# Kernel tuning notes

Hardware: AMD Instinct MI355X
Metric: run time of the kernel (lower is better)

Reference implementation:

```python
import jax, jax.numpy as jnp
import numpy as np

B, S, D = 4, 2048, 512
H, DK, DV = 8, 64, 64


def setup_inputs() -> dict:
    key = jax.random.key(0)
    ks = jax.random.split(key, 12)
    inv = 1.0 / np.sqrt(D)
    return {
        "query": jax.random.normal(ks[0], (B, S, D), dtype=jnp.float32),
        "value": jax.random.normal(ks[1], (B, S, D), dtype=jnp.float32),
        "attention_mask": jax.random.randint(ks[2], (B, S), 0, 2, dtype=jnp.int32),
        "Wq": jax.random.normal(ks[3], (D, H * DK), dtype=jnp.float32) * inv,
        "bq": jnp.zeros((H * DK,), dtype=jnp.float32),
        "Wk": jax.random.normal(ks[4], (D, H * DK), dtype=jnp.float32) * inv,
        "bk": jnp.zeros((H * DK,), dtype=jnp.float32),
        "Wv": jax.random.normal(ks[5], (D, H * DV), dtype=jnp.float32) * inv,
        "bv": jnp.zeros((H * DV,), dtype=jnp.float32),
        "Wo": jax.random.normal(ks[6], (H * DV, D), dtype=jnp.float32) * inv,
        "bo": jnp.zeros((D,), dtype=jnp.float32),
    }


def _split_heads(x, h):
    b, s, _ = x.shape
    return x.reshape(b, s, h, -1).transpose(0, 2, 1, 3)  # (B,H,S,dh)


def reference(query, value, attention_mask, Wq, bq, Wk, bk, Wv, bv, Wo, bo):
    # QKV projections (activation=None -> identity); key defaults to value
    q = _split_heads(query @ Wq + bq, H)   # (B,H,S,DK)
    k = _split_heads(value @ Wk + bk, H)   # (B,H,S,DK)
    v = _split_heads(value @ Wv + bv, H)   # (B,H,S,DV)

    scores = jnp.einsum("bhqd,bhkd->bhqk", q, k) / jnp.sqrt(jnp.float32(DK))
    # additive mask: m = 1e9*(mask-1), applied on both key and query axes
    m = 1e9 * (attention_mask.astype(jnp.float32) - 1.0)  # (B,S)
    scores = scores + m[:, None, None, :] + m[:, None, :, None]

    weights = jax.nn.softmax(scores, axis=-1)
    ctx = jnp.einsum("bhqk,bhkd->bhqd", weights, v)        # (B,H,S,DV)
    ctx = ctx.transpose(0, 2, 1, 3).reshape(ctx.shape[0], ctx.shape[2], H * DV)
    return ctx @ Wo + bo  # (B,S,D)
```

## Files before the change

### kernel.cpp

```cpp
#include <hip/hip_runtime.h>

#define B_ 4
#define S_ 2048
#define D_ 512
#define H_ 8

typedef __attribute__((ext_vector_type(8))) __bf16 bf16x8;
typedef __attribute__((ext_vector_type(4))) float f32x4;

#define NEGBIG  -1.442695040e9f
#define QSCALE  0.18033688011112042f

__device__ __forceinline__ unsigned pack_rn(float a, float b) {
    union { float f; unsigned u; } ua, ub; ua.f = a; ub.f = b;
    return __builtin_amdgcn_perm(ub.u + 0x8000u, ua.u + 0x8000u, 0x07060302u);
}

__device__ __forceinline__ void gl16(const void* g, void* l) {
    __builtin_amdgcn_global_load_lds(
        (const __attribute__((address_space(1))) unsigned int*)g,
        (__attribute__((address_space(3))) unsigned int*)l, 16, 0, 0);
}

__global__ __launch_bounds__(256) void pre_all(
    const float* __restrict__ q, const float* __restrict__ v,
    const int* __restrict__ am,
    const float* __restrict__ Wq, const float* __restrict__ Wk,
    const float* __restrict__ Wv, const float* __restrict__ Wo,
    unsigned short* __restrict__ xq, unsigned short* __restrict__ xv,
    unsigned short* __restrict__ Tq, unsigned short* __restrict__ Tk,
    unsigned short* __restrict__ Tv, unsigned short* __restrict__ To,
    int* __restrict__ idxc, int* __restrict__ nvout,
    float* __restrict__ Mf, float* __restrict__ Mc)
{
    const int bid = blockIdx.x;
    const int tid = threadIdx.x;

    if (bid < 4096) {
        const int z = bid >> 11, xb = bid & 2047;
        const float* src = z ? v : q;
        unsigned short* dst = z ? xv : xq;
        int i = (xb * 256 + tid) * 8;
        float4 f0 = *(const float4*)&src[i];
        float4 f1 = *(const float4*)&src[i + 4];
        uint4 o;
        o.x = pack_rn(f0.x, f0.y); o.y = pack_rn(f0.z, f0.w);
        o.z = pack_rn(f1.x, f1.y); o.w = pack_rn(f1.z, f1.w);
        *(uint4*)&dst[i] = o;
    } else if (bid < 4352) {
        int r = bid - 4096;
        int z = r >> 6, rem = r & 63;
        const float* W = (z == 0) ? Wq : (z == 1) ? Wk : (z == 2) ? Wv : Wo;
        unsigned short* T = (z == 0) ? Tq : (z == 1) ? Tk : (z == 2) ? Tv : To;
        int n0 = (rem & 7) * 64, k0 = (rem >> 3) * 64;

        __shared__ float Ts[64][69];
        #pragma unroll
        for (int it = 0; it < 4; it++) {
            int lin = tid + it * 256;
            int kr = lin >> 4, c4 = (lin & 15) * 4;
            float4 vv = *(const float4*)&W[(k0 + kr) * 512 + n0 + c4];
            Ts[kr][c4 + 0] = vv.x; Ts[kr][c4 + 1] = vv.y;
            Ts[kr][c4 + 2] = vv.z; Ts[kr][c4 + 3] = vv.w;
        }
        __syncthreads();
        int n = tid >> 2, kc = tid & 3;
        unsigned p[8];
        #pragma unroll
        for (int j = 0; j < 8; j++)
            p[j] = pack_rn(Ts[kc * 16 + 2 * j][n], Ts[kc * 16 + 2 * j + 1][n]);
        unsigned short* dst = &T[(n0 + n) * 512 + k0 + kc * 16];
        *(uint4*)dst       = *(uint4*)&p[0];
        *(uint4*)(dst + 8) = *(uint4*)&p[4];
    } else {
        const int w = tid >> 6, lane = tid & 63;
        const int* amb = am + w * 2048;
        int m[32];
        #pragma unroll
        for (int s = 0; s < 32; s++) m[s] = amb[s * 64 + lane];

        int* ib = idxc + w * 2048;
        const unsigned long long lt = (1ULL << lane) - 1ULL;
        int base = 0;
        #pragma unroll
        for (int s = 0; s < 32; s++) {
            unsigned long long bal = __ballot(m[s] != 0);
            if (m[s]) ib[base + __popcll(bal & lt)] = s * 64 + lane;
            base += __popcll(bal);
        }
        const int nv = base;
        for (int i = nv + lane; i < 2048; i += 64) ib[i] = 0;
        float* mfb = Mf + w * 2048;
        float* mcb = Mc + w * 2048;
        #pragma unroll
        for (int s = 0; s < 32; s++) {
            int i = s * 64 + lane;
            mfb[i] = m[s] ? 0.f : NEGBIG;
            mcb[i] = (i < nv) ? 0.f : NEGBIG;
        }
        if (lane == 0) nvout[w] = nv;
    }
}

__global__ __launch_bounds__(256) void proj_qkv_mfma(
    const unsigned short* __restrict__ Xq, const unsigned short* __restrict__ Xv,
    const unsigned short* __restrict__ Wtq, const unsigned short* __restrict__ Wtk,
    const unsigned short* __restrict__ Wtv,
    const float* __restrict__ bq, const float* __restrict__ bk,
    const float* __restrict__ bv,
    const int* __restrict__ idxc, const int* __restrict__ nv1,
    unsigned short* __restrict__ Qb, unsigned short* __restrict__ Kb,
    unsigned short* __restrict__ VtG)
{
    const int z = blockIdx.z;
    const unsigned short* A  = (z == 0) ? Wtq : (z == 1) ? Wtk : Xv;
    const unsigned short* Bm = (z == 0) ? Xq  : (z == 1) ? Xv  : Wtv;
    const float* bias        = (z == 0) ? bq  : (z == 1) ? bk  : bv;
    const int m0 = (z < 2) ? blockIdx.y * 128 : blockIdx.x * 128;
    const int n0 = (z < 2) ? blockIdx.x * 128 : blockIdx.y * 128;

    if (z == 1) {
        int bb = n0 >> 11, cap = (nv1[bb] + 127) & ~127;
        if (cap < 128) cap = 128;
        if ((n0 & 2047) >= cap) return;
    }
    if (z == 2) {
        int bb = m0 >> 11, cap = (nv1[bb] + 127) & ~127;
        if (cap < 128) cap = 128;
        if ((m0 & 2047) >= cap) return;
    }

    const int tid = threadIdx.x;
    const int w = tid >> 6, lane = tid & 63;
    const int l15 = lane & 15, quad = lane >> 4;
    const int wm = (w >> 1) * 64, wn = (w & 1) * 64;

    __shared__ unsigned short As[128 * 64];
    __shared__ unsigned short Bs[128 * 64];

    const int srw  = tid >> 3;
    const int csrc = (tid & 7) ^ (srw & 7);
    const unsigned short* aS[4];
    const unsigned short* bS[4];
    unsigned short* la[4];
    unsigned short* lb[4];
    #pragma unroll
    for (int is = 0; is < 4; is++) {
        int ra = m0 + is * 32 + srw;
        int rb = n0 + is * 32 + srw;
        long sa = ra, sb = rb;
        if (z == 2) { int bb = ra >> 11; sa = (long)bb * 2048 + idxc[bb * 2048 + (ra & 2047)]; }
        if (z == 1) { int bb = rb >> 11; sb = (long)bb * 2048 + idxc[bb * 2048 + (rb & 2047)]; }
        aS[is] = A  + sa * 512 + csrc * 8;
        bS[is] = Bm + sb * 512 + csrc * 8;
        la[is] = &As[is * 2048 + w * 512];
        lb[is] = &Bs[is * 2048 + w * 512];
    }

    const int koff0 = ((quad    ) ^ (l15 & 7)) * 8;
    const int koff1 = ((quad + 4) ^ (l15 & 7)) * 8;

    f32x4 acc[4][4];
    #pragma unroll
    for (int i = 0; i < 4; i++)
        #pragma unroll
        for (int j = 0; j < 4; j++) acc[i][j] = (f32x4){0.f, 0.f, 0.f, 0.f};

    for (int k0 = 0; k0 < 512; k0 += 64) {
        __syncthreads();
        #pragma unroll
        for (int is = 0; is < 4; is++) {
            gl16(aS[is] + k0, la[is]);
            gl16(bS[is] + k0, lb[is]);
        }
        __syncthreads();
        #pragma unroll
        for (int kc = 0; kc < 2; kc++) {
            const int ko = kc ? koff1 : koff0;
            bf16x8 a[4], bb[4];
            #pragma unroll
            for (int i = 0; i < 4; i++)
                a[i] = *(const bf16x8*)&As[(wm + 16 * i + l15) * 64 + ko];
            #pragma unroll
            for (int j = 0; j < 4; j++)
                bb[j] = *(const bf16x8*)&Bs[(wn + 16 * j + l15) * 64 + ko];
            #pragma unroll
            for (int i = 0; i < 4; i++)
                #pragma unroll
                for (int j = 0; j < 4; j++)
                    acc[i][j] = __builtin_amdgcn_mfma_f32_16x16x32_bf16(a[i], bb[j], acc[i][j], 0, 0, 0);
        }
    }

    if (z == 2) {
        #pragma unroll
        for (int j = 0; j < 4; j++) {
            int N = n0 + wn + 16 * j + l15;
            float bv_ = bias[N];
            int h = N >> 6, d = N & 63;
            #pragma unroll
            for (int i = 0; i < 4; i++) {
                int Mb = m0 + wm + 16 * i + quad * 4;
                int b = Mb >> 11, s = Mb & 2047;
                uint2 o;
                o.x = pack_rn(acc[i][j][0] + bv_, acc[i][j][1] + bv_);
                o.y = pack_rn(acc[i][j][2] + bv_, acc[i][j][3] + bv_);
                *(uint2*)&VtG[((b * H_ + h) * 64 + d) * 2048 + s] = o;
            }
        }
    } else {
        unsigned short* dst = (z == 0) ? Qb : Kb;
        const float scale = (z == 0) ? QSCALE : 1.0f;
        #pragma unroll
        for (int j = 0; j < 4; j++) {
            int sg = n0 + wn + 16 * j + l15;
            int b = sg >> 11, s = sg & 2047;
            #pragma unroll
            for (int i = 0; i < 4; i++) {
                int F = m0 + wm + 16 * i + quad * 4;
                int h = F >> 6, d = F & 63;
                float4 b4 = *(const float4*)&bias[F];
                uint2 o;
                o.x = pack_rn((acc[i][j][0] + b4.x) * scale, (acc[i][j][1] + b4.y) * scale);
                o.y = pack_rn((acc[i][j][2] + b4.z) * scale, (acc[i][j][3] + b4.w) * scale);
                *(uint2*)&dst[((b * H_ + h) * 2048 + s) * 64 + d] = o;
            }
        }
    }
}

__global__ __launch_bounds__(256, 2) void flash_mfma(
    const unsigned short* __restrict__ Qg, const unsigned short* __restrict__ Kg,
    const unsigned short* __restrict__ VtG, const float* __restrict__ Mf,
    const float* __restrict__ Mc, const int* __restrict__ nvalid,
    unsigned short* __restrict__ ctxB)
{
    const int bid = blockIdx.x;
    const int xcd = bid & 7, idx = bid >> 3;
    const int bh = xcd * 4 + (idx & 3);
    const int q0 = (idx >> 2) * 128;
    const int b = bh >> 3, h = bh & 7;

    const int tid = threadIdx.x;
    const int w = tid >> 6, lane = tid & 63;
    const int l15 = lane & 15, quad = lane >> 4;
    const int swz = l15 & 7;

    __shared__ unsigned short Ks[2][64 * 64];
    __shared__ unsigned short Ps[4][32 * 64];
    unsigned short* pw = &Ps[w][0];

    const int nv = nvalid[b];
    int ntiles = (nv + 63) >> 6;
    if (ntiles < 1) ntiles = 1;

    const float* mfb = Mf + b * 2048;
    const float* mcp = Mc + b * 2048 + quad * 4;

    bf16x8 qf[2][2];
    float mq[2];
    #pragma unroll
    for (int qb = 0; qb < 2; qb++) {
        int qrow = q0 + w * 32 + qb * 16 + l15;
        const unsigned short* p = &Qg[((long)bh * 2048 + qrow) * 64 + quad * 8];
        qf[qb][0] = *(const bf16x8*)p;
        qf[qb][1] = *(const bf16x8*)(p + 32);
        mq[qb] = mfb[qrow];
    }

    const unsigned short* vp[4];
    #pragma unroll
    for (int i = 0; i < 4; i++)
        vp[i] = VtG + ((long)bh * 64 + i * 16 + l15) * 2048 + quad * 8;

    const int srow = tid >> 2;
    const int sch  = (tid & 3) * 2;
    const unsigned short* kgb = Kg + (long)bh * 2048 * 64;
    const int sw0 = srow * 64 + ((sch    ) ^ (srow & 7)) * 8;
    const int sw1 = srow * 64 + ((sch + 1) ^ (srow & 7)) * 8;

    {
        uint4 a = *(const uint4*)&kgb[srow * 64 + sch * 8];
        uint4 c = *(const uint4*)&kgb[srow * 64 + sch * 8 + 8];
        *(uint4*)&Ks[0][sw0] = a;
        *(uint4*)&Ks[0][sw1] = c;
    }

    const int koff0 = ((quad    ) ^ swz) * 8;
    const int koff1 = ((quad + 4) ^ swz) * 8;

    f32x4 accO[2][4];
    #pragma unroll
    for (int qb = 0; qb < 2; qb++)
        #pragma unroll
        for (int dt = 0; dt < 4; dt++) accO[qb][dt] = (f32x4){0.f, 0.f, 0.f, 0.f};
    float mi[2] = {-3.0e38f, -3.0e38f};
    float li[2] = {0.f, 0.f};

    __syncthreads();

    for (int t = 0; t < ntiles; t++) {
        const int kt = t * 64;
        const int ktn = (t + 1 < ntiles) ? kt + 64 : kt;
        const int cur = t & 1, nxt = cur ^ 1;

        bf16x8 vf[4][2];
        #pragma unroll
        for (int dt = 0; dt < 4; dt++) {
            vf[dt][0] = *(const bf16x8*)(vp[dt] + kt);
            vf[dt][1] = *(const bf16x8*)(vp[dt] + kt + 32);
        }
        uint4 kst0 = *(const uint4*)&kgb[(ktn + srow) * 64 + sch * 8];
        uint4 kst1 = *(const uint4*)&kgb[(ktn + srow) * 64 + sch * 8 + 8];
        f32x4 kmf[4];
        #pragma unroll
        for (int nt = 0; nt < 4; nt++)
            kmf[nt] = *(const f32x4*)(mcp + kt + nt * 16);

        bf16x8 kf[4][2];
        #pragma unroll
        for (int nt = 0; nt < 4; nt++) {
            kf[nt][0] = *(const bf16x8*)&Ks[cur][(nt * 16 + l15) * 64 + koff0];
            kf[nt][1] = *(const bf16x8*)&Ks[cur][(nt * 16 + l15) * 64 + koff1];
        }
        f32x4 sc[2][4];
        #pragma unroll
        for (int qb = 0; qb < 2; qb++)
            #pragma unroll
            for (int nt = 0; nt < 4; nt++) {
                f32x4 c = kmf[nt];
                c[0] += mq[qb]; c[1] += mq[qb]; c[2] += mq[qb]; c[3] += mq[qb];
                sc[qb][nt] = c;
            }
        __builtin_amdgcn_s_setprio(1);
        #pragma unroll
        for (int qb = 0; qb < 2; qb++)
            #pragma unroll
            for (int nt = 0; nt < 4; nt++) {
                sc[qb][nt] = __builtin_amdgcn_mfma_f32_16x16x32_bf16(
                    kf[nt][0], qf[qb][0], sc[qb][nt], 0, 0, 0);
                sc[qb][nt] = __builtin_amdgcn_mfma_f32_16x16x32_bf16(
                    kf[nt][1], qf[qb][1], sc[qb][nt], 0, 0, 0);
            }
        __builtin_amdgcn_s_setprio(0);

        #pragma unroll
        for (int qb = 0; qb < 2; qb++) {
            float mloc = fmaxf(fmaxf(sc[qb][0][0], sc[qb][0][1]),
                               fmaxf(sc[qb][0][2], sc[qb][0][3]));
            #pragma unroll
            for (int nt = 1; nt < 4; nt++)
                mloc = fmaxf(mloc, fmaxf(fmaxf(sc[qb][nt][0], sc[qb][nt][1]),
                                         fmaxf(sc[qb][nt][2], sc[qb][nt][3])));
            mloc = fmaxf(mloc, __shfl_xor(mloc, 16));
            mloc = fmaxf(mloc, __shfl_xor(mloc, 32));

            float mn = mi[qb];
            if (!__all(mloc <= mn + 4.f)) {
                float mo = mn;
                mn = fmaxf(mo, mloc);
                float alpha = __builtin_amdgcn_exp2f(mo - mn);
                li[qb] *= alpha;
                #pragma unroll
                for (int dt = 0; dt < 4; dt++) {
                    accO[qb][dt][0] *= alpha; accO[qb][dt][1] *= alpha;
                    accO[qb][dt][2] *= alpha; accO[qb][dt][3] *= alpha;
                }
                mi[qb] = mn;
            }

            float ps = 0.f;
            const int prbase = (qb * 16 + l15) * 64;
            #pragma unroll
            for (int nt = 0; nt < 4; nt++) {
                float p0 = __builtin_amdgcn_exp2f(sc[qb][nt][0] - mn);
                float p1 = __builtin_amdgcn_exp2f(sc[qb][nt][1] - mn);
                float p2 = __builtin_amdgcn_exp2f(sc[qb][nt][2] - mn);
                float p3 = __builtin_amdgcn_exp2f(sc[qb][nt][3] - mn);
                ps += (p0 + p1) + (p2 + p3);
                uint2 pp;
                pp.x = pack_rn(p0, p1);
                pp.y = pack_rn(p2, p3);
                *(uint2*)&pw[prbase + ((2 * nt + (quad >> 1)) ^ swz) * 8 + (quad & 1) * 4] = pp;
            }
            ps += __shfl_xor(ps, 16);
            ps += __shfl_xor(ps, 32);
            li[qb] += ps;
        }

        #pragma unroll
        for (int qb = 0; qb < 2; qb++) {
            bf16x8 pf0 = *(const bf16x8*)&pw[(qb * 16 + l15) * 64 + koff0];
            bf16x8 pf1 = *(const bf16x8*)&pw[(qb * 16 + l15) * 64 + koff1];
            __builtin_amdgcn_s_setprio(1);
            #pragma unroll
            for (int dt = 0; dt < 4; dt++) {
                accO[qb][dt] = __builtin_amdgcn_mfma_f32_16x16x32_bf16(
                    vf[dt][0], pf0, accO[qb][dt], 0, 0, 0);
                accO[qb][dt] = __builtin_amdgcn_mfma_f32_16x16x32_bf16(
                    vf[dt][1], pf1, accO[qb][dt], 0, 0, 0);
            }
            __builtin_amdgcn_s_setprio(0);
        }

        *(uint4*)&Ks[nxt][sw0] = kst0;
        *(uint4*)&Ks[nxt][sw1] = kst1;
        __syncthreads();
    }

    #pragma unroll
    for (int qb = 0; qb < 2; qb++) {
        float inv = 1.f / li[qb];
        int q = q0 + w * 32 + qb * 16 + l15;
        int obase = (b * 2048 + q) * 512 + h * 64 + quad * 4;
        #pragma unroll
        for (int dt = 0; dt < 4; dt++) {
            uint2 o;
            o.x = pack_rn(accO[qb][dt][0] * inv, accO[qb][dt][1] * inv);
            o.y = pack_rn(accO[qb][dt][2] * inv, accO[qb][dt][3] * inv);
            *(uint2*)&ctxB[obase + dt * 16] = o;
        }
    }
}

__global__ __launch_bounds__(256) void proj_out_mfma(
    const unsigned short* __restrict__ ctxB, const unsigned short* __restrict__ Wto,
    const float* __restrict__ bo, float* __restrict__ out)
{
    const int m0 = blockIdx.y * 128, n0 = blockIdx.x * 128;
    const int tid = threadIdx.x;
    const int w = tid >> 6, lane = tid & 63;
    const int l15 = lane & 15, quad = lane >> 4;
    const int wm = (w >> 1) * 64, wn = (w & 1) * 64;

    __shared__ unsigned short As[128 * 64];
    __shared__ unsigned short Bs[128 * 64];

    const int srw  = tid >> 3;
    const int csrc = (tid & 7) ^ (srw & 7);
    const unsigned short* aS[4];
    const unsigned short* bS[4];
    unsigned short* la[4];
    unsigned short* lb[4];
    #pragma unroll
    for (int is = 0; is < 4; is++) {
        aS[is] = Wto  + (long)(m0 + is * 32 + srw) * 512 + csrc * 8;
        bS[is] = ctxB + (long)(n0 + is * 32 + srw) * 512 + csrc * 8;
        la[is] = &As[is * 2048 + w * 512];
        lb[is] = &Bs[is * 2048 + w * 512];
    }
    const int koff0 = ((quad    ) ^ (l15 & 7)) * 8;
    const int koff1 = ((quad + 4) ^ (l15 & 7)) * 8;

    f32x4 acc[4][4];
    #pragma unroll
    for (int i = 0; i < 4; i++)
        #pragma unroll
        for (int j = 0; j < 4; j++) acc[i][j] = (f32x4){0.f, 0.f, 0.f, 0.f};

    for (int k0 = 0; k0 < 512; k0 += 64) {
        __syncthreads();
        #pragma unroll
        for (int is = 0; is < 4; is++) {
            gl16(aS[is] + k0, la[is]);
            gl16(bS[is] + k0, lb[is]);
        }
        __syncthreads();
        #pragma unroll
        for (int kc = 0; kc < 2; kc++) {
            const int ko = kc ? koff1 : koff0;
            bf16x8 a[4], bb[4];
            #pragma unroll
            for (int i = 0; i < 4; i++)
                a[i] = *(const bf16x8*)&As[(wm + 16 * i + l15) * 64 + ko];
            #pragma unroll
            for (int j = 0; j < 4; j++)
                bb[j] = *(const bf16x8*)&Bs[(wn + 16 * j + l15) * 64 + ko];
            #pragma unroll
            for (int i = 0; i < 4; i++)
                #pragma unroll
                for (int j = 0; j < 4; j++)
                    acc[i][j] = __builtin_amdgcn_mfma_f32_16x16x32_bf16(a[i], bb[j], acc[i][j], 0, 0, 0);
        }
    }

    #pragma unroll
    for (int j = 0; j < 4; j++) {
        int sg = n0 + wn + 16 * j + l15;
        #pragma unroll
        for (int i = 0; i < 4; i++) {
            int F = m0 + wm + 16 * i + quad * 4;
            float4 b4 = *(const float4*)&bo[F];
            float4 vv;
            vv.x = acc[i][j][0] + b4.x;
            vv.y = acc[i][j][1] + b4.y;
            vv.z = acc[i][j][2] + b4.z;
            vv.w = acc[i][j][3] + b4.w;
            *(float4*)&out[sg * 512 + F] = vv;
        }
    }
}

extern "C" void kernel_launch(void* const* d_in, const int* in_sizes, int n_in,
                              void* d_out, int out_size, void* d_ws, size_t ws_size,
                              hipStream_t stream)
{
    const float* query = (const float*)d_in[0];
    const float* value = (const float*)d_in[1];
    const int*   amask = (const int*)d_in[2];
    const float* Wq = (const float*)d_in[3];
    const float* bq = (const float*)d_in[4];
    const float* Wk = (const float*)d_in[5];
    const float* bk = (const float*)d_in[6];
    const float* Wv = (const float*)d_in[7];
    const float* bv = (const float*)d_in[8];
    const float* Wo = (const float*)d_in[9];
    const float* bo = (const float*)d_in[10];
    float* out = (float*)d_out;

    char* ws = (char*)d_ws;
    const size_t MB = 1 << 20;
    const size_t KB = 1 << 10;
    unsigned short* Xbq = (unsigned short*)(ws);
    unsigned short* Xbv = (unsigned short*)(ws + 8 * MB);
    unsigned short* Wtq = (unsigned short*)(ws + 16 * MB);
    unsigned short* Wtk = (unsigned short*)(ws + 16 * MB + MB / 2);
    unsigned short* Wtv = (unsigned short*)(ws + 17 * MB);
    unsigned short* Wto = (unsigned short*)(ws + 17 * MB + MB / 2);
    unsigned short* Qb  = (unsigned short*)(ws + 18 * MB);
    unsigned short* Kb  = (unsigned short*)(ws + 26 * MB);
    unsigned short* VtG = (unsigned short*)(ws + 34 * MB);
    int*   idx1 = (int*)(ws + 42 * MB);
    float* Mf   = (float*)(ws + 42 * MB + 32 * KB);
    float* Mc   = (float*)(ws + 42 * MB + 64 * KB);
    int*   nv   = (int*)(ws + 42 * MB + 96 * KB);
    unsigned short* ctx = Xbq;

    pre_all<<<dim3(4353), 256, 0, stream>>>(query, value, amask,
                                            Wq, Wk, Wv, Wo,
                                            Xbq, Xbv, Wtq, Wtk, Wtv, Wto,
                                            idx1, nv, Mf, Mc);
    proj_qkv_mfma<<<dim3(64, 4, 3), 256, 0, stream>>>(Xbq, Xbv, Wtq, Wtk, Wtv,
                                                      bq, bk, bv, idx1, nv,
                                                      Qb, Kb, VtG);
    flash_mfma<<<dim3(512), 256, 0, stream>>>(Qb, Kb, VtG, Mf, Mc, nv, ctx);
    proj_out_mfma<<<dim3(64, 4), 256, 0, stream>>>(ctx, Wto, bo, out);
}
```

Before: 187.6 us.

## Double-buffer projection GEMM LDS tiles and shrink N tile to 64

Both projection GEMMs switch from single-buffered LDS staging with two syncthreads per K step to a double-buffered pipeline, where the next K slab is prefetched while the current one is computed and explicit vmcnt waits plus barriers replace the syncs. The N tile is halved to 64, doubling the grid so more blocks run across CUs, and the masked-row skip is tightened to 64-row granularity. In exchange each block gets less data reuse per byte loaded and LDS use per block rises from the double buffers.

```diff
diff --git a/kernel.cpp b/kernel.cpp
--- a/kernel.cpp
+++ b/kernel.cpp
@@ -116,85 +116,100 @@
     const unsigned short* A  = (z == 0) ? Wtq : (z == 1) ? Wtk : Xv;
     const unsigned short* Bm = (z == 0) ? Xq  : (z == 1) ? Xv  : Wtv;
     const float* bias        = (z == 0) ? bq  : (z == 1) ? bk  : bv;
-    const int m0 = (z < 2) ? blockIdx.y * 128 : blockIdx.x * 128;
-    const int n0 = (z < 2) ? blockIdx.x * 128 : blockIdx.y * 128;
+    const int lin0 = blockIdx.y * 128 + blockIdx.x;
+    const int m0 = (z < 2) ? blockIdx.y * 128 : (lin0 >> 3) * 128;
+    const int n0 = (z < 2) ? blockIdx.x * 64  : (lin0 & 7) * 64;
 
     if (z == 1) {
-        int bb = n0 >> 11, cap = (nv1[bb] + 127) & ~127;
-        if (cap < 128) cap = 128;
+        int bb = n0 >> 11, cap = (nv1[bb] + 63) & ~63;
+        if (cap < 64) cap = 64;
         if ((n0 & 2047) >= cap) return;
     }
     if (z == 2) {
-        int bb = m0 >> 11, cap = (nv1[bb] + 127) & ~127;
-        if (cap < 128) cap = 128;
+        int bb = m0 >> 11, cap = (nv1[bb] + 63) & ~63;
+        if (cap < 64) cap = 64;
         if ((m0 & 2047) >= cap) return;
     }
 
     const int tid = threadIdx.x;
     const int w = tid >> 6, lane = tid & 63;
     const int l15 = lane & 15, quad = lane >> 4;
-    const int wm = (w >> 1) * 64, wn = (w & 1) * 64;
-
-    __shared__ unsigned short As[128 * 64];
-    __shared__ unsigned short Bs[128 * 64];
+    const int wm = (w >> 1) * 64, wn = (w & 1) * 32;
+
+    __shared__ unsigned short As[2][128 * 64];
+    __shared__ unsigned short Bs[2][64 * 64];
 
     const int srw  = tid >> 3;
     const int csrc = (tid & 7) ^ (srw & 7);
     const unsigned short* aS[4];
-    const unsigned short* bS[4];
-    unsigned short* la[4];
-    unsigned short* lb[4];
+    const unsigned short* bS[2];
     #pragma unroll
     for (int is = 0; is < 4; is++) {
         int ra = m0 + is * 32 + srw;
+        long sa = ra;
+        if (z == 2) { int bb = ra >> 11; sa = (long)bb * 2048 + idxc[bb * 2048 + (ra & 2047)]; }
+        aS[is] = A + sa * 512 + csrc * 8;
+    }
+    #pragma unroll
+    for (int is = 0; is < 2; is++) {
         int rb = n0 + is * 32 + srw;
-        long sa = ra, sb = rb;
-        if (z == 2) { int bb = ra >> 11; sa = (long)bb * 2048 + idxc[bb * 2048 + (ra & 2047)]; }
+        long sb = rb;
         if (z == 1) { int bb = rb >> 11; sb = (long)bb * 2048 + idxc[bb * 2048 + (rb & 2047)]; }
-        aS[is] = A  + sa * 512 + csrc * 8;
         bS[is] = Bm + sb * 512 + csrc * 8;
-        la[is] = &As[is * 2048 + w * 512];
-        lb[is] = &Bs[is * 2048 + w * 512];
     }
 
     const int koff0 = ((quad    ) ^ (l15 & 7)) * 8;
     const int koff1 = ((quad + 4) ^ (l15 & 7)) * 8;
 
-    f32x4 acc[4][4];
+    f32x4 acc[4][2];
     #pragma unroll
     for (int i = 0; i < 4; i++)
         #pragma unroll
-        for (int j = 0; j < 4; j++) acc[i][j] = (f32x4){0.f, 0.f, 0.f, 0.f};
-
-    for (int k0 = 0; k0 < 512; k0 += 64) {
-        __syncthreads();
-        #pragma unroll
-        for (int is = 0; is < 4; is++) {
-            gl16(aS[is] + k0, la[is]);
-            gl16(bS[is] + k0, lb[is]);
-        }
-        __syncthreads();
+        for (int j = 0; j < 2; j++) acc[i][j] = (f32x4){0.f, 0.f, 0.f, 0.f};
+
+    #define STAGE_Q(buf, k0)                                        \
+        do {                                                        \
+            _Pragma("unroll")                                       \
+            for (int is = 0; is < 4; is++)                          \
+                gl16(aS[is] + (k0), &As[buf][is * 2048 + w * 512]); \
+            _Pragma("unroll")                                       \
+            for (int is = 0; is < 2; is++)                          \
+                gl16(bS[is] + (k0), &Bs[buf][is * 2048 + w * 512]); \
+        } while (0)
+
+    STAGE_Q(0, 0);
+    for (int k = 0; k < 8; k++) {
+        const int cur = k & 1;
+        if (k < 7) {
+            STAGE_Q(cur ^ 1, (k + 1) * 64);
+            asm volatile("s_waitcnt vmcnt(6)" ::: "memory");
+        } else {
+            asm volatile("s_waitcnt vmcnt(0)" ::: "memory");
+        }
+        asm volatile("s_barrier" ::: "memory");
         #pragma unroll
         for (int kc = 0; kc < 2; kc++) {
             const int ko = kc ? koff1 : koff0;
-            bf16x8 a[4], bb[4];
+            bf16x8 a[4], bb[2];
             #pragma unroll
             for (int i = 0; i < 4; i++)
-                a[i] = *(const bf16x8*)&As[(wm + 16 * i + l15) * 64 + ko];
-            #pragma unroll
-            for (int j = 0; j < 4; j++)
-                bb[j] = *(const bf16x8*)&Bs[(wn + 16 * j + l15) * 64 + ko];
+                a[i] = *(const bf16x8*)&As[cur][(wm + 16 * i + l15) * 64 + ko];
+            #pragma unroll
+            for (int j = 0; j < 2; j++)
+                bb[j] = *(const bf16x8*)&Bs[cur][(wn + 16 * j + l15) * 64 + ko];
             #pragma unroll
             for (int i = 0; i < 4; i++)
                 #pragma unroll
-                for (int j = 0; j < 4; j++)
+                for (int j = 0; j < 2; j++)
                     acc[i][j] = __builtin_amdgcn_mfma_f32_16x16x32_bf16(a[i], bb[j], acc[i][j], 0, 0, 0);
         }
-    }
+        asm volatile("s_barrier" ::: "memory");
+    }
+    #undef STAGE_Q
 
     if (z == 2) {
         #pragma unroll
-        for (int j = 0; j < 4; j++) {
+        for (int j = 0; j < 2; j++) {
             int N = n0 + wn + 16 * j + l15;
             float bv_ = bias[N];
             int h = N >> 6, d = N & 63;
@@ -212,7 +227,7 @@
         unsigned short* dst = (z == 0) ? Qb : Kb;
         const float scale = (z == 0) ? QSCALE : 1.0f;
         #pragma unroll
-        for (int j = 0; j < 4; j++) {
+        for (int j = 0; j < 2; j++) {
             int sg = n0 + wn + 16 * j + l15;
             int b = sg >> 11, s = sg & 2047;
             #pragma unroll
@@ -427,65 +442,77 @@
     const unsigned short* __restrict__ ctxB, const unsigned short* __restrict__ Wto,
     const float* __restrict__ bo, float* __restrict__ out)
 {
-    const int m0 = blockIdx.y * 128, n0 = blockIdx.x * 128;
+    const int m0 = blockIdx.y * 128, n0 = blockIdx.x * 64;
     const int tid = threadIdx.x;
     const int w = tid >> 6, lane = tid & 63;
     const int l15 = lane & 15, quad = lane >> 4;
-    const int wm = (w >> 1) * 64, wn = (w & 1) * 64;
-
-    __shared__ unsigned short As[128 * 64];
-    __shared__ unsigned short Bs[128 * 64];
+    const int wm = (w >> 1) * 64, wn = (w & 1) * 32;
+
+    __shared__ unsigned short As[2][128 * 64];
+    __shared__ unsigned short Bs[2][64 * 64];
 
     const int srw  = tid >> 3;
     const int csrc = (tid & 7) ^ (srw & 7);
     const unsigned short* aS[4];
-    const unsigned short* bS[4];
-    unsigned short* la[4];
-    unsigned short* lb[4];
-    #pragma unroll
-    for (int is = 0; is < 4; is++) {
+    const unsigned short* bS[2];
+    #pragma unroll
+    for (int is = 0; is < 4; is++)
         aS[is] = Wto  + (long)(m0 + is * 32 + srw) * 512 + csrc * 8;
+    #pragma unroll
+    for (int is = 0; is < 2; is++)
         bS[is] = ctxB + (long)(n0 + is * 32 + srw) * 512 + csrc * 8;
-        la[is] = &As[is * 2048 + w * 512];
-        lb[is] = &Bs[is * 2048 + w * 512];
-    }
+
     const int koff0 = ((quad    ) ^ (l15 & 7)) * 8;
     const int koff1 = ((quad + 4) ^ (l15 & 7)) * 8;
 
-    f32x4 acc[4][4];
+    f32x4 acc[4][2];
     #pragma unroll
     for (int i = 0; i < 4; i++)
         #pragma unroll
-        for (int j = 0; j < 4; j++) acc[i][j] = (f32x4){0.f, 0.f, 0.f, 0.f};
-
-    for (int k0 = 0; k0 < 512; k0 += 64) {
-        __syncthreads();
-        #pragma unroll
-        for (int is = 0; is < 4; is++) {
-            gl16(aS[is] + k0, la[is]);
-            gl16(bS[is] + k0, lb[is]);
-        }
-        __syncthreads();
+        for (int j = 0; j < 2; j++) acc[i][j] = (f32x4){0.f, 0.f, 0.f, 0.f};
+
+    #define STAGE_O(buf, k0)                                        \
+        do {                                                        \
+            _Pragma("unroll")                                       \
+            for (int is = 0; is < 4; is++)                          \
+                gl16(aS[is] + (k0), &As[buf][is * 2048 + w * 512]); \
+            _Pragma("unroll")                                       \
+            for (int is = 0; is < 2; is++)                          \
+                gl16(bS[is] + (k0), &Bs[buf][is * 2048 + w * 512]); \
+        } while (0)
+
+    STAGE_O(0, 0);
+    for (int k = 0; k < 8; k++) {
+        const int cur = k & 1;
+        if (k < 7) {
+            STAGE_O(cur ^ 1, (k + 1) * 64);
+            asm volatile("s_waitcnt vmcnt(6)" ::: "memory");
+        } else {
+            asm volatile("s_waitcnt vmcnt(0)" ::: "memory");
+        }
+        asm volatile("s_barrier" ::: "memory");
         #pragma unroll
         for (int kc = 0; kc < 2; kc++) {
             const int ko = kc ? koff1 : koff0;
-            bf16x8 a[4], bb[4];
+            bf16x8 a[4], bb[2];
             #pragma unroll
             for (int i = 0; i < 4; i++)
-                a[i] = *(const bf16x8*)&As[(wm + 16 * i + l15) * 64 + ko];
-            #pragma unroll
-            for (int j = 0; j < 4; j++)
-                bb[j] = *(const bf16x8*)&Bs[(wn + 16 * j + l15) * 64 + ko];
+                a[i] = *(const bf16x8*)&As[cur][(wm + 16 * i + l15) * 64 + ko];
+            #pragma unroll
+            for (int j = 0; j < 2; j++)
+                bb[j] = *(const bf16x8*)&Bs[cur][(wn + 16 * j + l15) * 64 + ko];
             #pragma unroll
             for (int i = 0; i < 4; i++)
                 #pragma unroll
-                for (int j = 0; j < 4; j++)
+                for (int j = 0; j < 2; j++)
                     acc[i][j] = __builtin_amdgcn_mfma_f32_16x16x32_bf16(a[i], bb[j], acc[i][j], 0, 0, 0);
         }
-    }
-
-    #pragma unroll
-    for (int j = 0; j < 4; j++) {
+        asm volatile("s_barrier" ::: "memory");
+    }
+    #undef STAGE_O
+
+    #pragma unroll
+    for (int j = 0; j < 2; j++) {
         int sg = n0 + wn + 16 * j + l15;
         #pragma unroll
         for (int i = 0; i < 4; i++) {
@@ -540,9 +567,9 @@
                                             Wq, Wk, Wv, Wo,
                                             Xbq, Xbv, Wtq, Wtk, Wtv, Wto,
                                             idx1, nv, Mf, Mc);
-    proj_qkv_mfma<<<dim3(64, 4, 3), 256, 0, stream>>>(Xbq, Xbv, Wtq, Wtk, Wtv,
-                                                      bq, bk, bv, idx1, nv,
-                                                      Qb, Kb, VtG);
+    proj_qkv_mfma<<<dim3(128, 4, 3), 256, 0, stream>>>(Xbq, Xbv, Wtq, Wtk, Wtv,
+                                                       bq, bk, bv, idx1, nv,
+                                                       Qb, Kb, VtG);
     flash_mfma<<<dim3(512), 256, 0, stream>>>(Qb, Kb, VtG, Mf, Mc, nv, ctx);
-    proj_out_mfma<<<dim3(64, 4), 256, 0, stream>>>(ctx, Wto, bo, out);
-}
+    proj_out_mfma<<<dim3(128, 4), 256, 0, stream>>>(ctx, Wto, bo, out);
+}
```

Measured after the change: 182.8 us. -2.6%, faster.
